# Kernel tuning notes

Measured on AMD Instinct MI355X. Metric: run time of the kernel, lower is better.

Reference implementation:

```python
import jax, jax.numpy as jnp
import numpy as np

BRANCH = 16   # children per internal node
DEPTH = 4     # levels 0..4, leaves at level 4
IN = 512
HID = 512

def _level_sizes():
    return [BRANCH ** d for d in range(DEPTH + 1)]

def setup_inputs() -> dict:
    key = jax.random.key(0)
    ks = jax.random.split(key, 9)
    N = sum(_level_sizes())  # 69905
    x = jax.random.normal(ks[0], (N, IN), dtype=jnp.float32)
    s = 1.0 / np.sqrt(IN + HID)  # torch nn.Linear default init bound
    def lin(kw, kb):
        w = jax.random.uniform(kw, (HID, IN + HID), jnp.float32, -s, s)
        b = jax.random.uniform(kb, (HID,), jnp.float32, -s, s)
        return w, b
    wi_w, wi_b = lin(ks[1], ks[2])
    wf_w, wf_b = lin(ks[3], ks[4])
    wo_w, wo_b = lin(ks[5], ks[6])
    wu_w, wu_b = lin(ks[7], ks[8])
    return {"x": x, "wi_w": wi_w, "wi_b": wi_b, "wf_w": wf_w, "wf_b": wf_b,
            "wo_w": wo_w, "wo_b": wo_b, "wu_w": wu_w, "wu_b": wu_b}

def reference(x, wi_w, wi_b, wf_w, wf_b, wo_w, wo_b, wu_w, wu_b):
    sizes = _level_sizes()
    offs = np.concatenate([[0], np.cumsum(sizes)])
    levels = [x[offs[d]:offs[d + 1]] for d in range(DEPTH + 1)]

    def gates(xh):
        i = jax.nn.sigmoid(xh @ wi_w.T + wi_b)
        o = jax.nn.sigmoid(xh @ wo_w.T + wo_b)
        u = jnp.tanh(xh @ wu_w.T + wu_b)
        return i, o, u

    # leaf_forward: h_prev = 0, no forget terms
    Xl = levels[DEPTH]
    xh = jnp.concatenate([Xl, jnp.zeros((Xl.shape[0], HID), Xl.dtype)], axis=1)
    i, o, u = gates(xh)
    C = i * u
    H = o * jnp.tanh(C)

    # node_forward, bottom-up. Faithful quirk of the source: the forget gate
    # is computed on the child CELL state (cat(x, c_k)), not the hidden state.
    for d in range(DEPTH - 1, -1, -1):
        Xd = levels[d]                      # [n, IN]
        n = Xd.shape[0]
        Hc = H.reshape(n, BRANCH, HID)      # children hidden
        Cc = C.reshape(n, BRANCH, HID)      # children cell
        h_sum = Hc.sum(axis=1)
        xh = jnp.concatenate([Xd, h_sum], axis=1)
        i, o, u = gates(xh)
        xc = jnp.concatenate([jnp.broadcast_to(Xd[:, None, :], (n, BRANCH, IN)), Cc], axis=-1)
        f = jax.nn.sigmoid(jnp.einsum('nbk,hk->nbh', xc, wf_w) + wf_b)
        C = i * u + (f * Cc).sum(axis=1)
        H = o * jnp.tanh(C)

    return H[0], C[0]
```

## Files before the change

### kernel.cpp

```cpp
#include <hip/hip_runtime.h>
#include <stdint.h>
#include <stddef.h>


typedef __bf16 bf16x8 __attribute__((ext_vector_type(8)));
typedef float  f32x4  __attribute__((ext_vector_type(4)));
typedef void __attribute__((address_space(3))) lds_void_t;
typedef void __attribute__((address_space(1))) gbl_void_t;

__device__ __forceinline__ uint16_t f2bf(float f) {
  union { __bf16 b; uint16_t u; } v;
  v.b = (__bf16)f;
  return v.u;
}
__device__ __forceinline__ float bf2f(uint16_t u) {
  union { uint32_t u; float f; } v; v.u = (uint32_t)u << 16;
  return v.f;
}
__device__ __forceinline__ float sig_(float x) {
  return __builtin_amdgcn_rcpf(1.0f + __expf(-x));
}
__device__ __forceinline__ float tanh_(float x) {
  return __builtin_fmaf(2.f,
      __builtin_amdgcn_rcpf(1.f + __expf(-2.f * x)), -1.f);
}

__global__ void k_conv_all(const float4* __restrict__ x,
                           ushort4* __restrict__ xdst, long n4x,
                           const float4* __restrict__ w0,
                           const float4* __restrict__ w1,
                           const float4* __restrict__ w2,
                           const float4* __restrict__ w3,
                           ushort4* __restrict__ wdst) {
  const long per4 = (long)512 * 1024 / 4;
  const long total = n4x + 4 * per4;
  long i = blockIdx.x * (long)blockDim.x + threadIdx.x;
  long stride = (long)gridDim.x * blockDim.x;
  for (; i < total; i += stride) {
    float4 v;
    ushort4* d;
    if (i < n4x) {
      v = x[i];
      d = xdst + i;
    } else {
      long j = i - n4x;
      long seg = j / per4, off2 = j - seg * per4;
      const float4* s = (seg == 0) ? w0 : (seg == 1) ? w1
                       : (seg == 2) ? w2 : w3;
      v = s[off2];
      d = wdst + j;
    }
    ushort4 r;
    r.x = f2bf(v.x); r.y = f2bf(v.y); r.z = f2bf(v.z); r.w = f2bf(v.w);
    *d = r;
  }
}

#define BM 128
#define BN 128
#define BK 32

__global__ __launch_bounds__(256, 3)
void k_leaf_fx(const uint16_t* __restrict__ Xleaf,
               const uint16_t* __restrict__ Wg,
               const float* __restrict__ bi, const float* __restrict__ bo,
               const float* __restrict__ bu,
               uint16_t* __restrict__ Cbf,
               const uint16_t* __restrict__ Xnext,
               uint16_t* __restrict__ xh_next,
               const uint16_t* __restrict__ Xbf,
               const uint16_t* __restrict__ Wf,
               float* __restrict__ FxAll) {
  __shared__ uint16_t smem[20480];
  const int tid = threadIdx.x, lane = tid & 63, wave = tid >> 6;
  const int lrow = lane & 15, quad = lane >> 4;

  if (blockIdx.x < 4096) {
    uint16_t* As = smem;
    uint16_t* Bs = smem + 8192;
    const int wm = (wave >> 1) * 64, wn = (wave & 1) * 32;
    long tm, tn;
    {
      int b = blockIdx.x;
      int x = b & 7, j = b >> 3, per = 64;
      tn = j & 7; tm = (long)x * per + (j >> 3);
    }
    f32x4 acc[3][4][2] = {};
    const int srow = lane >> 3;
    const int scol = (((lane & 7) ^ srow) << 3);
    const int rsw = lrow & 7;
    const int pc[2] = { ((0 + quad) ^ rsw) << 3, ((4 + quad) ^ rsw) << 3 };

    for (int k0 = 0; k0 < 512; k0 += 64) {
#pragma unroll
      for (int j = 0; j < 4; ++j) {
        int grp = wave * 4 + j;
        int row = grp * 8 + srow;
        const uint16_t* gp = Xleaf + (tm * 128 + row) * 512L + k0 + scol;
        __builtin_amdgcn_global_load_lds((gbl_void_t*)(uintptr_t)gp,
            (lds_void_t*)&As[grp * 512], 16, 0, 0);
      }
#pragma unroll
      for (int j = 0; j < 6; ++j) {
        int cc = wave * 6 + j;
        int g  = cc >> 3;
        long grow = (long)g * 512 + tn * 64 + (cc & 7) * 8 + srow;
        const uint16_t* gp = Wg + grow * 1024 + k0 + scol;
        __builtin_amdgcn_global_load_lds((gbl_void_t*)(uintptr_t)gp,
            (lds_void_t*)&Bs[cc * 512], 16, 0, 0);
      }
      __syncthreads();
#pragma unroll
      for (int h = 0; h < 2; ++h) {
        bf16x8 a[4];
#pragma unroll
        for (int f = 0; f < 4; ++f)
          a[f] = *(const bf16x8*)&As[(wm + f * 16 + lrow) * 64 + pc[h]];
#pragma unroll
        for (int g = 0; g < 3; ++g) {
          bf16x8 b0 = *(const bf16x8*)&Bs[(g * 64 + wn + lrow) * 64 + pc[h]];
          bf16x8 b1 = *(const bf16x8*)&Bs[(g * 64 + wn + 16 + lrow) * 64 +
                                          pc[h]];
#pragma unroll
          for (int fm = 0; fm < 4; ++fm) {
            acc[g][fm][0] = __builtin_amdgcn_mfma_f32_16x16x32_bf16(
                a[fm], b0, acc[g][fm][0], 0, 0, 0);
            acc[g][fm][1] = __builtin_amdgcn_mfma_f32_16x16x32_bf16(
                a[fm], b1, acc[g][fm][1], 0, 0, 0);
          }
        }
      }
      __syncthreads();
    }
#pragma unroll
    for (int fn = 0; fn < 2; ++fn) {
      long col = tn * 64 + wn + fn * 16 + lrow;
      float biv = bi[col], bov = bo[col], buv = bu[col];
#pragma unroll
      for (int fm = 0; fm < 4; ++fm) {
        long row0 = tm * 128 + wm + fm * 16 + quad * 4;
        long pg   = tm * 8 + (wm >> 4) + fm;
        float hs = 0.f;
#pragma unroll
        for (int r = 0; r < 4; ++r) {
          long row = row0 + r;
          float iv = sig_(acc[0][fm][fn][r] + biv);
          float ov = sig_(acc[1][fm][fn][r] + bov);
          float uv = tanh_(acc[2][fm][fn][r] + buv);
          float c  = iv * uv;
          Cbf[row * 512 + col] = f2bf(c);
          hs += ov * tanh_(c);
        }
        hs += __shfl_xor(hs, 16, 64);
        hs += __shfl_xor(hs, 32, 64);
        if (quad == 0) {
          xh_next[pg * 1024 + col]       = Xnext[pg * 512 + col];
          xh_next[pg * 1024 + 512 + col] = f2bf(hs);
        }
      }
    }
  } else {
    uint16_t* As = smem;
    uint16_t* Bs = smem + 4096;
    const int wm = (wave >> 1) * 64, wn = (wave & 1) * 64;
    int bid2 = (int)blockIdx.x - 4096;
    const long tm = bid2 % 35, tn = bid2 / 35;
    f32x4 acc[4][4] = {};
    const int srow2 = lane >> 2, scol2 = (lane & 3) * 8;
    for (int k0 = 0; k0 < 512; k0 += BK) {
#pragma unroll
      for (int i = 0; i < 2; ++i) {
        int row = i * 64 + wave * 16 + srow2;
        const uint16_t* gp = Xbf + (tm * BM + row) * 512L + k0 + scol2;
        __builtin_amdgcn_global_load_lds((gbl_void_t*)(uintptr_t)gp,
            (lds_void_t*)&As[i * 2048 + wave * 512], 16, 0, 0);
      }
#pragma unroll
      for (int i = 0; i < 2; ++i) {
        int row = i * 64 + wave * 16 + srow2;
        const uint16_t* gp = Wf + (tn * BN + row) * 1024L + k0 + scol2;
        __builtin_amdgcn_global_load_lds((gbl_void_t*)(uintptr_t)gp,
            (lds_void_t*)&Bs[i * 2048 + wave * 512], 16, 0, 0);
      }
      __syncthreads();
      bf16x8 a[4], b[4];
#pragma unroll
      for (int f = 0; f < 4; ++f)
        a[f] = *(const bf16x8*)&As[(wm + f * 16 + lrow) * BK + quad * 8];
#pragma unroll
      for (int f = 0; f < 4; ++f)
        b[f] = *(const bf16x8*)&Bs[(wn + f * 16 + lrow) * BK + quad * 8];
#pragma unroll
      for (int fm = 0; fm < 4; ++fm)
#pragma unroll
        for (int fn = 0; fn < 4; ++fn)
          acc[fm][fn] = __builtin_amdgcn_mfma_f32_16x16x32_bf16(
              a[fm], b[fn], acc[fm][fn], 0, 0, 0);
      __syncthreads();
    }
#pragma unroll
    for (int fm = 0; fm < 4; ++fm)
#pragma unroll
      for (int fn = 0; fn < 4; ++fn) {
        long col  = tn * BN + wn + fn * 16 + lrow;
        long row0 = tm * BM + wm + fm * 16 + quad * 4;
#pragma unroll
        for (int r = 0; r < 4; ++r)
          FxAll[(row0 + r) * 512 + col] = acc[fm][fn][r];
      }
  }
}

__global__ __launch_bounds__(256, 3)
void k_fc4_l3g(const uint16_t* __restrict__ Cbf,
               const uint16_t* __restrict__ Wfc,
               const float* __restrict__ Fx,
               const float* __restrict__ bfb,
               float* __restrict__ Fpart,
               const uint16_t* __restrict__ xhA,
               const uint16_t* __restrict__ Wg,
               float* __restrict__ G3) {
  __shared__ uint16_t smem[16384];
  const int tid = threadIdx.x, lane = tid & 63, wave = tid >> 6;
  const int lrow = lane & 15, quad = lane >> 4;
  const int srow = lane >> 3;
  const int scol = (((lane & 7) ^ srow) << 3);
  const int rsw = lrow & 7;
  const int pc[2] = { ((0 + quad) ^ rsw) << 3, ((4 + quad) ^ rsw) << 3 };

  if (blockIdx.x < 2048) {
    uint16_t* As = smem;
    uint16_t* Bs = smem + 8192;
    const int wm = (wave >> 1) * 64, wn = (wave & 1) * 64;
    long tm, tn;
    {
      int b = blockIdx.x;
      int x = b & 7, j = b >> 3, per = 64;
      tn = j & 3; tm = (long)x * per + (j >> 2);
    }
    f32x4 acc[4][4] = {};
    for (int k0 = 0; k0 < 512; k0 += 64) {
#pragma unroll
      for (int j = 0; j < 4; ++j) {
        int grp = wave * 4 + j;
        int row = grp * 8 + srow;
        const uint16_t* gp = Cbf + (tm * 128 + row) * 512L + k0 + scol;
        __builtin_amdgcn_global_load_lds((gbl_void_t*)(uintptr_t)gp,
            (lds_void_t*)&As[grp * 512], 16, 0, 0);
      }
#pragma unroll
      for (int j = 0; j < 4; ++j) {
        int row = wave * 32 + j * 8 + srow;
        const uint16_t* gp = Wfc + (tn * BN + row) * 1024L + k0 + scol;
        __builtin_amdgcn_global_load_lds((gbl_void_t*)(uintptr_t)gp,
            (lds_void_t*)&Bs[(wave * 32 + j * 8) * 64], 16, 0, 0);
      }
      __syncthreads();
#pragma unroll
      for (int h = 0; h < 2; ++h) {
        bf16x8 a[4], b[4];
#pragma unroll
        for (int f = 0; f < 4; ++f)
          a[f] = *(const bf16x8*)&As[(wm + f * 16 + lrow) * 64 + pc[h]];
#pragma unroll
        for (int f = 0; f < 4; ++f)
          b[f] = *(const bf16x8*)&Bs[(wn + f * 16 + lrow) * 64 + pc[h]];
#pragma unroll
        for (int fm = 0; fm < 4; ++fm)
#pragma unroll
          for (int fn = 0; fn < 4; ++fn)
            acc[fm][fn] = __builtin_amdgcn_mfma_f32_16x16x32_bf16(
                a[fm], b[fn], acc[fm][fn], 0, 0, 0);
      }
      __syncthreads();
    }
#pragma unroll
    for (int fm = 0; fm < 4; ++fm) {
      long pg   = tm * 8 + (wm >> 4) + fm;
      long row0 = tm * 128 + wm + fm * 16 + quad * 4;
#pragma unroll
      for (int fn = 0; fn < 4; ++fn) {
        long col = tn * BN + wn + fn * 16 + lrow;
        float fx = Fx[pg * 512 + col] + bfb[col];
        float t = 0.f;
#pragma unroll
        for (int r = 0; r < 4; ++r)
          t += sig_(fx + acc[fm][fn][r]) * bf2f(Cbf[(row0 + r) * 512 + col]);
        t += __shfl_xor(t, 16, 64);
        t += __shfl_xor(t, 32, 64);
        if (quad == 0) Fpart[pg * 512 + col] = t;
      }
    }
  } else {
    uint16_t* As = smem;
    uint16_t* Bs = smem + 4096;
    const int wm = (wave >> 1) * 32, wn = (wave & 1) * 32;
    long tm, tn;
    {
      int b = (int)blockIdx.x - 2048;
      int x = b & 7, j = b >> 3, per = 8;
      tn = j & 7; tm = (long)x * per + (j >> 3);
    }
    f32x4 acc[3][2][2] = {};
    for (int k0 = 0; k0 < 1024; k0 += 64) {
#pragma unroll
      for (int j = 0; j < 2; ++j) {
        int grp = wave * 2 + j;
        int row = grp * 8 + srow;
        const uint16_t* gp = xhA + (tm * 64 + row) * 1024L + k0 + scol;
        __builtin_amdgcn_global_load_lds((gbl_void_t*)(uintptr_t)gp,
            (lds_void_t*)&As[grp * 512], 16, 0, 0);
      }
#pragma unroll
      for (int j = 0; j < 6; ++j) {
        int cc = wave * 6 + j;
        int g  = cc >> 3;
        long grow = (long)g * 512 + tn * 64 + (cc & 7) * 8 + srow;
        const uint16_t* gp = Wg + grow * 1024 + k0 + scol;
        __builtin_amdgcn_global_load_lds((gbl_void_t*)(uintptr_t)gp,
            (lds_void_t*)&Bs[cc * 512], 16, 0, 0);
      }
      __syncthreads();
#pragma unroll
      for (int h = 0; h < 2; ++h) {
        bf16x8 a[2];
#pragma unroll
        for (int f = 0; f < 2; ++f)
          a[f] = *(const bf16x8*)&As[(wm + f * 16 + lrow) * 64 + pc[h]];
#pragma unroll
        for (int g = 0; g < 3; ++g) {
          bf16x8 b0 = *(const bf16x8*)&Bs[(g * 64 + wn + lrow) * 64 + pc[h]];
          bf16x8 b1 = *(const bf16x8*)&Bs[(g * 64 + wn + 16 + lrow) * 64 +
                                          pc[h]];
#pragma unroll
          for (int fm = 0; fm < 2; ++fm) {
            acc[g][fm][0] = __builtin_amdgcn_mfma_f32_16x16x32_bf16(
                a[fm], b0, acc[g][fm][0], 0, 0, 0);
            acc[g][fm][1] = __builtin_amdgcn_mfma_f32_16x16x32_bf16(
                a[fm], b1, acc[g][fm][1], 0, 0, 0);
          }
        }
      }
      __syncthreads();
    }
#pragma unroll
    for (int fn = 0; fn < 2; ++fn) {
      long col = tn * 64 + wn + fn * 16 + lrow;
#pragma unroll
      for (int fm = 0; fm < 2; ++fm) {
        long row0 = tm * 64 + wm + fm * 16 + quad * 4;
#pragma unroll
        for (int r = 0; r < 4; ++r) {
          long row = row0 + r;
#pragma unroll
          for (int g = 0; g < 3; ++g)
            G3[row * 1536 + g * 512 + col] = acc[g][fm][fn][r];
        }
      }
    }
  }
}

__global__ void k_level_final(const float* __restrict__ G3,
                              const float* __restrict__ Fpart,
                              const float* __restrict__ bi,
                              const float* __restrict__ bo,
                              const float* __restrict__ bu,
                              uint16_t* __restrict__ Cbf_out,
                              const uint16_t* __restrict__ Xnext,
                              uint16_t* __restrict__ xh_next) {
  const long p = blockIdx.x;
  const int hq = (threadIdx.x & 127) << 2;
  float4 b_i = *(const float4*)(bi + hq);
  float4 b_o = *(const float4*)(bo + hq);
  float4 b_u = *(const float4*)(bu + hq);
  const float* bip = &b_i.x; const float* bop = &b_o.x;
  const float* bup = &b_u.x;
  float hs[4] = {0.f, 0.f, 0.f, 0.f};
#pragma unroll 4
  for (int k = 0; k < 16; ++k) {
    long row = p * 16 + k;
    float4 gi = *(const float4*)(G3 + row * 1536 + hq);
    float4 go = *(const float4*)(G3 + row * 1536 + 512 + hq);
    float4 gu = *(const float4*)(G3 + row * 1536 + 1024 + hq);
    float4 fp = *(const float4*)(Fpart + row * 512 + hq);
    const float* gip = &gi.x; const float* gop = &go.x;
    const float* gup = &gu.x; const float* fpp = &fp.x;
    ushort4 cw; unsigned short* cwp = &cw.x;
#pragma unroll
    for (int j = 0; j < 4; ++j) {
      float iv = sig_(gip[j] + bip[j]);
      float ov = sig_(gop[j] + bop[j]);
      float uv = tanh_(gup[j] + bup[j]);
      float c  = iv * uv + fpp[j];
      cwp[j] = f2bf(c);
      hs[j] += ov * tanh_(c);
    }
    *(ushort4*)(Cbf_out + row * 512 + hq) = cw;
  }
  *(ushort4*)(xh_next + p * 1024 + hq) = *(const ushort4*)(Xnext + p * 512 + hq);
  ushort4 hw = {f2bf(hs[0]), f2bf(hs[1]), f2bf(hs[2]), f2bf(hs[3])};
  *(ushort4*)(xh_next + p * 1024 + 512 + hq) = hw;
}

__global__ __launch_bounds__(256, 3)
void k_fc2_l2g(const uint16_t* __restrict__ CbfU,
               const uint16_t* __restrict__ Wfc,
               const float* __restrict__ Fx,
               const float* __restrict__ bfb,
               float* __restrict__ Fpart,
               const uint16_t* __restrict__ xhB,
               const uint16_t* __restrict__ Wg,
               float* __restrict__ G3) {
  __shared__ uint16_t smem[16384];
  const int tid = threadIdx.x, lane = tid & 63, wave = tid >> 6;
  const int lrow = lane & 15, quad = lane >> 4;
  const int srow = lane >> 3;
  const int scol = (((lane & 7) ^ srow) << 3);
  const int rsw = lrow & 7;
  const int pc[2] = { ((0 + quad) ^ rsw) << 3, ((4 + quad) ^ rsw) << 3 };

  if (blockIdx.x < 256) {
    uint16_t* As = smem;
    uint16_t* Bs = smem + 4096;
    const int wm = (wave >> 1) * 32, wn = (wave & 1) * 64;
    long tm, tn;
    {
      int b = blockIdx.x;
      int x = b & 7, j = b >> 3, per = 8;
      tn = j & 3; tm = (long)x * per + (j >> 2);
    }
    f32x4 acc[2][4] = {};
    for (int k0 = 0; k0 < 512; k0 += 64) {
#pragma unroll
      for (int j = 0; j < 2; ++j) {
        int grp = wave * 2 + j;
        int row = grp * 8 + srow;
        const uint16_t* gp = CbfU + (tm * 64 + row) * 512L + k0 + scol;
        __builtin_amdgcn_global_load_lds((gbl_void_t*)(uintptr_t)gp,
            (lds_void_t*)&As[grp * 512], 16, 0, 0);
      }
#pragma unroll
      for (int j = 0; j < 4; ++j) {
        int row = wave * 32 + j * 8 + srow;
        const uint16_t* gp = Wfc + (tn * BN + row) * 1024L + k0 + scol;
        __builtin_amdgcn_global_load_lds((gbl_void_t*)(uintptr_t)gp,
            (lds_void_t*)&Bs[(wave * 32 + j * 8) * 64], 16, 0, 0);
      }
      __syncthreads();
#pragma unroll
      for (int h = 0; h < 2; ++h) {
        bf16x8 a[2], b[4];
#pragma unroll
        for (int f = 0; f < 2; ++f)
          a[f] = *(const bf16x8*)&As[(wm + f * 16 + lrow) * 64 + pc[h]];
#pragma unroll
        for (int f = 0; f < 4; ++f)
          b[f] = *(const bf16x8*)&Bs[(wn + f * 16 + lrow) * 64 + pc[h]];
#pragma unroll
        for (int fm = 0; fm < 2; ++fm)
#pragma unroll
          for (int fn = 0; fn < 4; ++fn)
            acc[fm][fn] = __builtin_amdgcn_mfma_f32_16x16x32_bf16(
                a[fm], b[fn], acc[fm][fn], 0, 0, 0);
      }
      __syncthreads();
    }
#pragma unroll
    for (int fm = 0; fm < 2; ++fm) {
      long pg   = tm * 4 + (wm >> 4) + fm;
      long row0 = tm * 64 + wm + fm * 16 + quad * 4;
#pragma unroll
      for (int fn = 0; fn < 4; ++fn) {
        long col = tn * BN + wn + fn * 16 + lrow;
        float fx = Fx[pg * 512 + col] + bfb[col];
        float t = 0.f;
#pragma unroll
        for (int r = 0; r < 4; ++r)
          t += sig_(fx + acc[fm][fn][r]) * bf2f(CbfU[(row0 + r) * 512 + col]);
        t += __shfl_xor(t, 16, 64);
        t += __shfl_xor(t, 32, 64);
        if (quad == 0) Fpart[pg * 512 + col] = t;
      }
    }
  } else {
    uint16_t* As = smem;
    uint16_t* Bs = smem + 4096;
    const int wm = (wave >> 1) * 32, wn = (wave & 1) * 32;
    int b = (int)blockIdx.x - 256;
    long tm = b >> 3, tn = b & 7;
    f32x4 acc[3][2][2] = {};
    for (int k0 = 0; k0 < 1024; k0 += 64) {
#pragma unroll
      for (int j = 0; j < 2; ++j) {
        int grp = wave * 2 + j;
        int row = grp * 8 + srow;
        const uint16_t* gp = xhB + (tm * 64 + row) * 1024L + k0 + scol;
        __builtin_amdgcn_global_load_lds((gbl_void_t*)(uintptr_t)gp,
            (lds_void_t*)&As[grp * 512], 16, 0, 0);
      }
#pragma unroll
      for (int j = 0; j < 6; ++j) {
        int cc = wave * 6 + j;
        int g  = cc >> 3;
        long grow = (long)g * 512 + tn * 64 + (cc & 7) * 8 + srow;
        const uint16_t* gp = Wg + grow * 1024 + k0 + scol;
        __builtin_amdgcn_global_load_lds((gbl_void_t*)(uintptr_t)gp,
            (lds_void_t*)&Bs[cc * 512], 16, 0, 0);
      }
      __syncthreads();
#pragma unroll
      for (int h = 0; h < 2; ++h) {
        bf16x8 a[2];
#pragma unroll
        for (int f = 0; f < 2; ++f)
          a[f] = *(const bf16x8*)&As[(wm + f * 16 + lrow) * 64 + pc[h]];
#pragma unroll
        for (int g = 0; g < 3; ++g) {
          bf16x8 b0 = *(const bf16x8*)&Bs[(g * 64 + wn + lrow) * 64 + pc[h]];
          bf16x8 b1 = *(const bf16x8*)&Bs[(g * 64 + wn + 16 + lrow) * 64 +
                                          pc[h]];
#pragma unroll
          for (int fm = 0; fm < 2; ++fm) {
            acc[g][fm][0] = __builtin_amdgcn_mfma_f32_16x16x32_bf16(
                a[fm], b0, acc[g][fm][0], 0, 0, 0);
            acc[g][fm][1] = __builtin_amdgcn_mfma_f32_16x16x32_bf16(
                a[fm], b1, acc[g][fm][1], 0, 0, 0);
          }
        }
      }
      __syncthreads();
    }
#pragma unroll
    for (int fn = 0; fn < 2; ++fn) {
      long col = tn * 64 + wn + fn * 16 + lrow;
#pragma unroll
      for (int fm = 0; fm < 2; ++fm) {
        long row0 = tm * 64 + wm + fm * 16 + quad * 4;
#pragma unroll
        for (int r = 0; r < 4; ++r) {
          long row = row0 + r;
#pragma unroll
          for (int g = 0; g < 3; ++g)
            G3[row * 1536 + g * 512 + col] = acc[g][fm][fn][r];
        }
      }
    }
  }
}

__global__ __launch_bounds__(256)
void k_fcdot(const uint16_t* __restrict__ Cbf,
             const uint16_t* __restrict__ Wfc,
             const float* __restrict__ Fx,
             const float* __restrict__ bfb,
             float* __restrict__ Fpart,
             const uint16_t* __restrict__ xhC,
             const uint16_t* __restrict__ Wg,
             float* __restrict__ Gf) {
  __shared__ uint16_t smem[12288];
  const int tid = threadIdx.x, lane = tid & 63, wave = tid >> 6;
  if (blockIdx.x < 16) {
    uint16_t* As = smem;
    uint16_t* Bs = smem + 4096;
    const int lrow = lane & 15, quad = lane >> 4;
    const int wm = (wave >> 1) * 32, wn = (wave & 1) * 64;
    int b = blockIdx.x;
    long tm = b >> 2, tn = b & 3;
    f32x4 acc[2][4] = {};
    const int srow = lane >> 3;
    const int scol = (((lane & 7) ^ srow) << 3);
    const int rsw = lrow & 7;
    const int pc[2] = { ((0 + quad) ^ rsw) << 3, ((4 + quad) ^ rsw) << 3 };
    for (int k0 = 0; k0 < 512; k0 += 64) {
#pragma unroll
      for (int j = 0; j < 2; ++j) {
        int grp = wave * 2 + j;
        int row = grp * 8 + srow;
        const uint16_t* gp = Cbf + (tm * 64 + row) * 512L + k0 + scol;
        __builtin_amdgcn_global_load_lds((gbl_void_t*)(uintptr_t)gp,
            (lds_void_t*)&As[grp * 512], 16, 0, 0);
      }
#pragma unroll
      for (int j = 0; j < 4; ++j) {
        int row = wave * 32 + j * 8 + srow;
        const uint16_t* gp = Wfc + (tn * 128 + row) * 1024L + k0 + scol;
        __builtin_amdgcn_global_load_lds((gbl_void_t*)(uintptr_t)gp,
            (lds_void_t*)&Bs[(wave * 32 + j * 8) * 64], 16, 0, 0);
      }
      __syncthreads();
#pragma unroll
      for (int h = 0; h < 2; ++h) {
        bf16x8 a[2], bb[4];
#pragma unroll
        for (int f = 0; f < 2; ++f)
          a[f] = *(const bf16x8*)&As[(wm + f * 16 + lrow) * 64 + pc[h]];
#pragma unroll
        for (int f = 0; f < 4; ++f)
          bb[f] = *(const bf16x8*)&Bs[(wn + f * 16 + lrow) * 64 + pc[h]];
#pragma unroll
        for (int fm = 0; fm < 2; ++fm)
#pragma unroll
          for (int fn = 0; fn < 4; ++fn)
            acc[fm][fn] = __builtin_amdgcn_mfma_f32_16x16x32_bf16(
                a[fm], bb[fn], acc[fm][fn], 0, 0, 0);
      }
      __syncthreads();
    }
#pragma unroll
    for (int fm = 0; fm < 2; ++fm) {
      long pg   = tm * 4 + (wm >> 4) + fm;
      long row0 = tm * 64 + wm + fm * 16 + quad * 4;
#pragma unroll
      for (int fn = 0; fn < 4; ++fn) {
        long col = tn * 128 + wn + fn * 16 + lrow;
        float fx = Fx[pg * 512 + col] + bfb[col];
        float t = 0.f;
#pragma unroll
        for (int r = 0; r < 4; ++r)
          t += sig_(fx + acc[fm][fn][r]) * bf2f(Cbf[(row0 + r) * 512 + col]);
        t += __shfl_xor(t, 16, 64);
        t += __shfl_xor(t, 32, 64);
        if (quad == 0) Fpart[pg * 512 + col] = t;
      }
    }
  } else {
    int wid = (int)(((long)(blockIdx.x - 16) * 256 + tid) >> 6);
    if (wid >= 16 * 1536) return;
    int m = wid / 1536, n = wid - m * 1536;
    const uint16_t* a = xhC + (long)m * 1024;
    const uint16_t* b = Wg + (long)n * 1024;
    int k0 = lane * 16;
    float s = 0.f;
#pragma unroll
    for (int j = 0; j < 16; j += 4) {
      ushort4 av = *(const ushort4*)(a + k0 + j);
      ushort4 bv = *(const ushort4*)(b + k0 + j);
      s += bf2f(av.x) * bf2f(bv.x) + bf2f(av.y) * bf2f(bv.y)
         + bf2f(av.z) * bf2f(bv.z) + bf2f(av.w) * bf2f(bv.w);
    }
#pragma unroll
    for (int off = 32; off; off >>= 1) s += __shfl_xor(s, off, 64);
    if (lane == 0) Gf[(long)m * 1536 + n] = s;
  }
}

__global__ void k_dot_merge(const uint16_t* __restrict__ xhC,
                            const uint16_t* __restrict__ Wg,
                            float* __restrict__ Gf,
                            const float* __restrict__ CupA,
                            const float* __restrict__ WfF,
                            float* __restrict__ Fc) {
  int wid  = (int)((blockIdx.x * (long)blockDim.x + threadIdx.x) >> 6);
  int lane = threadIdx.x & 63;
  if (wid < 1536) {
    const uint16_t* a = xhC;
    const uint16_t* b = Wg + (long)wid * 1024;
    int k0 = lane * 16;
    float s = 0.f;
#pragma unroll
    for (int j = 0; j < 16; j += 4) {
      ushort4 av = *(const ushort4*)(a + k0 + j);
      ushort4 bv = *(const ushort4*)(b + k0 + j);
      s += bf2f(av.x) * bf2f(bv.x) + bf2f(av.y) * bf2f(bv.y)
         + bf2f(av.z) * bf2f(bv.z) + bf2f(av.w) * bf2f(bv.w);
    }
#pragma unroll
    for (int off = 32; off; off >>= 1) s += __shfl_xor(s, off, 64);
    if (lane == 0) Gf[wid] = s;
  } else {
    int w2 = wid - 1536;
    if (w2 >= 16 * 512) return;
    int m = w2 >> 9, n = w2 & 511;
    const float* a = CupA + (long)m * 512;
    const float* b = WfF + (long)n * 1024;
    int k0 = lane * 8;
    float s = 0.f;
#pragma unroll
    for (int j = 0; j < 8; j += 4) {
      float4 av = *(const float4*)(a + k0 + j);
      float4 bv = *(const float4*)(b + k0 + j);
      s += av.x * bv.x + av.y * bv.y + av.z * bv.z + av.w * bv.w;
    }
#pragma unroll
    for (int off = 32; off; off >>= 1) s += __shfl_xor(s, off, 64);
    if (lane == 0) Fc[(long)m * 512 + n] = s;
  }
}

__global__ __launch_bounds__(1024)
void k_lvl1_tail(const float* __restrict__ G,
                 const float* __restrict__ Fpart,
                 const float* __restrict__ bi,
                 const float* __restrict__ bo,
                 const float* __restrict__ bu,
                 float* __restrict__ Cv,
                 const uint16_t* __restrict__ xroot,
                 uint16_t* __restrict__ xh) {
  __shared__ float Hl[16 * 512];
  const int tid = threadIdx.x;
#pragma unroll
  for (int it = 0; it < 2; ++it) {
    int idx = it * 1024 + tid;
    int p = idx >> 7, hq = (idx & 127) << 2;
    const float* g = G + (long)p * 1536;
    float4 gi = *(const float4*)(g + hq);
    float4 go = *(const float4*)(g + 512 + hq);
    float4 gu = *(const float4*)(g + 1024 + hq);
    float4 b_i = *(const float4*)(bi + hq);
    float4 b_o = *(const float4*)(bo + hq);
    float4 b_u = *(const float4*)(bu + hq);
    float4 fp = *(const float4*)(Fpart + (long)p * 512 + hq);
    const float* gip = &gi.x; const float* gop = &go.x;
    const float* gup = &gu.x; const float* bip = &b_i.x;
    const float* bop = &b_o.x; const float* bup = &b_u.x;
    const float* fpp = &fp.x;
    float4 hv, cv;
    float* hvp = &hv.x; float* cvp = &cv.x;
#pragma unroll
    for (int j = 0; j < 4; ++j) {
      float iv = sig_(gip[j] + bip[j]);
      float ov = sig_(gop[j] + bop[j]);
      float uv = tanh_(gup[j] + bup[j]);
      float c  = iv * uv + fpp[j];
      cvp[j] = c;
      hvp[j] = ov * tanh_(c);
    }
    *(float4*)(Cv + (long)p * 512 + hq) = cv;
    *(float4*)(&Hl[p * 512 + hq]) = hv;
  }
  __syncthreads();
  if (tid < 128) {
    int hq = tid << 2;
    float4 s = {0.f, 0.f, 0.f, 0.f};
#pragma unroll
    for (int b = 0; b < 16; ++b) {
      float4 v = *(const float4*)(&Hl[b * 512 + hq]);
      s.x += v.x; s.y += v.y; s.z += v.z; s.w += v.w;
    }
    *(ushort4*)(xh + hq) = *(const ushort4*)(xroot + hq);
    ushort4 hw = {f2bf(s.x), f2bf(s.y), f2bf(s.z), f2bf(s.w)};
    *(ushort4*)(xh + 512 + hq) = hw;
  }
}

__global__ void k_root_tail(const float* __restrict__ Fc,
                            const float* __restrict__ Fx,
                            const float* __restrict__ bfb,
                            const float* __restrict__ Cc,
                            const float* __restrict__ G,
                            const float* __restrict__ bi,
                            const float* __restrict__ bo,
                            const float* __restrict__ bu,
                            float* __restrict__ H, float* __restrict__ Cv) {
  int hq = (threadIdx.x & 127) << 2;
  float4 fxv = *(const float4*)(Fx + hq);
  float4 bfv = *(const float4*)(bfb + hq);
  float fx0 = fxv.x + bfv.x, fx1 = fxv.y + bfv.y;
  float fx2 = fxv.z + bfv.z, fx3 = fxv.w + bfv.w;
  float a0 = 0.f, a1 = 0.f, a2 = 0.f, a3 = 0.f;
#pragma unroll 4
  for (int b = 0; b < 16; ++b) {
    float4 f = *(const float4*)(Fc + (long)b * 512 + hq);
    float4 c = *(const float4*)(Cc + (long)b * 512 + hq);
    a0 += sig_(fx0 + f.x) * c.x;
    a1 += sig_(fx1 + f.y) * c.y;
    a2 += sig_(fx2 + f.z) * c.z;
    a3 += sig_(fx3 + f.w) * c.w;
  }
  float fpp[4] = {a0, a1, a2, a3};
  float4 gi = *(const float4*)(G + hq);
  float4 go = *(const float4*)(G + 512 + hq);
  float4 gu = *(const float4*)(G + 1024 + hq);
  float4 b_i = *(const float4*)(bi + hq);
  float4 b_o = *(const float4*)(bo + hq);
  float4 b_u = *(const float4*)(bu + hq);
  const float* gip = &gi.x; const float* gop = &go.x; const float* gup = &gu.x;
  const float* bip = &b_i.x; const float* bop = &b_o.x; const float* bup = &b_u.x;
  float4 hv, cv;
  float* hvp = &hv.x; float* cvp = &cv.x;
#pragma unroll
  for (int j = 0; j < 4; ++j) {
    float iv = sig_(gip[j] + bip[j]);
    float ov = sig_(gop[j] + bop[j]);
    float uv = tanh_(gup[j] + bup[j]);
    float c  = iv * uv + fpp[j];
    cvp[j] = c;
    hvp[j] = ov * tanh_(c);
  }
  *(float4*)(H  + hq) = hv;
  *(float4*)(Cv + hq) = cv;
}

extern "C" void kernel_launch(void* const* d_in, const int* in_sizes, int n_in,
                              void* d_out, int out_size, void* d_ws, size_t ws_size,
                              hipStream_t stream) {
  const float* x    = (const float*)d_in[0];
  const float* wi_w = (const float*)d_in[1];
  const float* wi_b = (const float*)d_in[2];
  const float* wf_w = (const float*)d_in[3];
  const float* wf_b = (const float*)d_in[4];
  const float* wo_w = (const float*)d_in[5];
  const float* wo_b = (const float*)d_in[6];
  const float* wu_w = (const float*)d_in[7];
  const float* wu_b = (const float*)d_in[8];
  (void)in_sizes; (void)n_in; (void)out_size; (void)ws_size;

  static const long offs[5] = {0, 1, 17, 273, 4369};
  const long NTOT = 69905;

  char* ws = (char*)d_ws;
  size_t off = 0;
  auto alloc = [&](size_t bytes) -> void* {
    void* p = ws + off;
    off += (bytes + 255) & ~(size_t)255;
    return p;
  };
  uint16_t* Xbf   = (uint16_t*)alloc(NTOT * 512 * 2);
  uint16_t* Wgw   = (uint16_t*)alloc((size_t)2048 * 1024 * 2);
  uint16_t* Wg    = Wgw;
  uint16_t* Wf    = Wgw + (size_t)1536 * 1024;
  float*    FxAll = (float*)alloc((size_t)4480 * 512 * 4);
  uint16_t* Cbf   = (uint16_t*)alloc((size_t)65536 * 512 * 2);
  uint16_t* CbfU  = (uint16_t*)alloc((size_t)4096 * 512 * 2);
  uint16_t* CbfU2 = (uint16_t*)alloc((size_t)256 * 512 * 2);
  uint16_t* xhA   = (uint16_t*)alloc((size_t)4096 * 1024 * 2);
  uint16_t* xhB   = (uint16_t*)alloc((size_t)256 * 1024 * 2);
  uint16_t* xhC   = (uint16_t*)alloc((size_t)16 * 1024 * 2);
  float*    Fpart = (float*)alloc((size_t)4096 * 512 * 4);
  float*    G3    = (float*)alloc((size_t)4096 * 1536 * 4);
  float*    Gf    = (float*)alloc((size_t)16 * 1536 * 4);
  float*    Fc    = (float*)alloc((size_t)16 * 512 * 4);
  float*    CupA  = (float*)alloc((size_t)16 * 512 * 4);

  {
    long n4x = NTOT * 512 / 4;
    k_conv_all<<<8192, 256, 0, stream>>>(
        (const float4*)x, (ushort4*)Xbf, n4x,
        (const float4*)wi_w, (const float4*)wo_w,
        (const float4*)wu_w, (const float4*)wf_w, (ushort4*)Wgw);
  }

  k_leaf_fx<<<4236, 256, 0, stream>>>(
      Xbf + offs[4] * 512, Wg, wi_b, wo_b, wu_b,
      Cbf, Xbf + offs[3] * 512, xhA,
      Xbf, Wf, FxAll);

  k_fc4_l3g<<<2560, 256, 0, stream>>>(
      Cbf, Wf + 512, FxAll + offs[3] * 512, wf_b, Fpart,
      xhA, Wg, G3);

  k_level_final<<<256, 128, 0, stream>>>(
      G3, Fpart, wi_b, wo_b, wu_b, CbfU, Xbf + offs[2] * 512, xhB);

  k_fc2_l2g<<<288, 256, 0, stream>>>(
      CbfU, Wf + 512, FxAll + offs[2] * 512, wf_b, Fpart,
      xhB, Wg, G3);

  k_level_final<<<16, 128, 0, stream>>>(
      G3, Fpart, wi_b, wo_b, wu_b, CbfU2, Xbf + offs[1] * 512, xhC);

  k_fcdot<<<6160, 256, 0, stream>>>(CbfU2, Wf + 512,
                                    FxAll + offs[1] * 512, wf_b, Fpart,
                                    xhC, Wg, Gf);

  k_lvl1_tail<<<1, 1024, 0, stream>>>(Gf, Fpart, wi_b, wo_b, wu_b,
                                      CupA, Xbf + offs[0] * 512, xhC);

  {
    long waves = 1536 + 16L * 512;
    k_dot_merge<<<(int)(waves / 4), 256, 0, stream>>>(
        xhC, Wg, Gf, CupA, wf_w + 512, Fc);
  }
  k_root_tail<<<1, 128, 0, stream>>>(Fc, FxAll, wf_b, CupA, Gf,
                                     wi_b, wo_b, wu_b,
                                     (float*)d_out, (float*)d_out + 512);
}
```

Before: 473.1 us.

## Fuse upper tree levels into one persistent kernel with grid barriers

Replaces the chain of eight small kernels for levels 3..0 with a single persistent kernel of 768 blocks. Software grid barriers built on atomics separate the phases, and each phase's work is distributed over the blocks in grid-stride form. This is meant to remove the launch overhead and tail idle time between the many tiny dependent kernels. In exchange it adds barrier spin costs, and it relies on all 768 blocks being co-resident under a normal launch. If they are not, the barrier can deadlock, though the spin limit eventually breaks the wait.

```diff
diff --git a/kernel.cpp b/kernel.cpp
--- a/kernel.cpp
+++ b/kernel.cpp
@@ -23,6 +23,32 @@
 __device__ __forceinline__ float tanh_(float x) {
   return __builtin_fmaf(2.f,
       __builtin_amdgcn_rcpf(1.f + __expf(-2.f * x)), -1.f);
+}
+
+#define NBLK 768u
+__device__ __forceinline__ void gbar(unsigned* bar) {
+  __syncthreads();
+  if (threadIdx.x == 0) {
+    __threadfence();
+    unsigned g = __hip_atomic_load(bar + 1, __ATOMIC_RELAXED,
+                                   __HIP_MEMORY_SCOPE_AGENT);
+    unsigned a = __hip_atomic_fetch_add(bar, 1u, __ATOMIC_ACQ_REL,
+                                        __HIP_MEMORY_SCOPE_AGENT) + 1u;
+    if (a == NBLK) {
+      __hip_atomic_store(bar, 0u, __ATOMIC_RELAXED, __HIP_MEMORY_SCOPE_AGENT);
+      __hip_atomic_fetch_add(bar + 1, 1u, __ATOMIC_RELEASE,
+                             __HIP_MEMORY_SCOPE_AGENT);
+    } else {
+      long spins = 0;
+      while (__hip_atomic_load(bar + 1, __ATOMIC_ACQUIRE,
+                               __HIP_MEMORY_SCOPE_AGENT) == g) {
+        if (++spins > (1L << 28)) break;
+        __builtin_amdgcn_s_sleep(8);
+      }
+    }
+    __threadfence();
+  }
+  __syncthreads();
 }
 
 __global__ void k_conv_all(const float4* __restrict__ x,
@@ -211,166 +237,34 @@
   }
 }
 
-__global__ __launch_bounds__(256, 3)
-void k_fc4_l3g(const uint16_t* __restrict__ Cbf,
-               const uint16_t* __restrict__ Wfc,
-               const float* __restrict__ Fx,
-               const float* __restrict__ bfb,
-               float* __restrict__ Fpart,
-               const uint16_t* __restrict__ xhA,
-               const uint16_t* __restrict__ Wg,
-               float* __restrict__ G3) {
-  __shared__ uint16_t smem[16384];
-  const int tid = threadIdx.x, lane = tid & 63, wave = tid >> 6;
-  const int lrow = lane & 15, quad = lane >> 4;
-  const int srow = lane >> 3;
-  const int scol = (((lane & 7) ^ srow) << 3);
-  const int rsw = lrow & 7;
-  const int pc[2] = { ((0 + quad) ^ rsw) << 3, ((4 + quad) ^ rsw) << 3 };
-
-  if (blockIdx.x < 2048) {
-    uint16_t* As = smem;
-    uint16_t* Bs = smem + 8192;
-    const int wm = (wave >> 1) * 64, wn = (wave & 1) * 64;
-    long tm, tn;
-    {
-      int b = blockIdx.x;
-      int x = b & 7, j = b >> 3, per = 64;
-      tn = j & 3; tm = (long)x * per + (j >> 2);
-    }
-    f32x4 acc[4][4] = {};
-    for (int k0 = 0; k0 < 512; k0 += 64) {
-#pragma unroll
-      for (int j = 0; j < 4; ++j) {
-        int grp = wave * 4 + j;
-        int row = grp * 8 + srow;
-        const uint16_t* gp = Cbf + (tm * 128 + row) * 512L + k0 + scol;
-        __builtin_amdgcn_global_load_lds((gbl_void_t*)(uintptr_t)gp,
-            (lds_void_t*)&As[grp * 512], 16, 0, 0);
-      }
-#pragma unroll
-      for (int j = 0; j < 4; ++j) {
-        int row = wave * 32 + j * 8 + srow;
-        const uint16_t* gp = Wfc + (tn * BN + row) * 1024L + k0 + scol;
-        __builtin_amdgcn_global_load_lds((gbl_void_t*)(uintptr_t)gp,
-            (lds_void_t*)&Bs[(wave * 32 + j * 8) * 64], 16, 0, 0);
-      }
-      __syncthreads();
-#pragma unroll
-      for (int h = 0; h < 2; ++h) {
-        bf16x8 a[4], b[4];
-#pragma unroll
-        for (int f = 0; f < 4; ++f)
-          a[f] = *(const bf16x8*)&As[(wm + f * 16 + lrow) * 64 + pc[h]];
-#pragma unroll
-        for (int f = 0; f < 4; ++f)
-          b[f] = *(const bf16x8*)&Bs[(wn + f * 16 + lrow) * 64 + pc[h]];
-#pragma unroll
-        for (int fm = 0; fm < 4; ++fm)
-#pragma unroll
-          for (int fn = 0; fn < 4; ++fn)
-            acc[fm][fn] = __builtin_amdgcn_mfma_f32_16x16x32_bf16(
-                a[fm], b[fn], acc[fm][fn], 0, 0, 0);
-      }
-      __syncthreads();
-    }
-#pragma unroll
-    for (int fm = 0; fm < 4; ++fm) {
-      long pg   = tm * 8 + (wm >> 4) + fm;
-      long row0 = tm * 128 + wm + fm * 16 + quad * 4;
-#pragma unroll
-      for (int fn = 0; fn < 4; ++fn) {
-        long col = tn * BN + wn + fn * 16 + lrow;
-        float fx = Fx[pg * 512 + col] + bfb[col];
-        float t = 0.f;
-#pragma unroll
-        for (int r = 0; r < 4; ++r)
-          t += sig_(fx + acc[fm][fn][r]) * bf2f(Cbf[(row0 + r) * 512 + col]);
-        t += __shfl_xor(t, 16, 64);
-        t += __shfl_xor(t, 32, 64);
-        if (quad == 0) Fpart[pg * 512 + col] = t;
-      }
-    }
-  } else {
-    uint16_t* As = smem;
-    uint16_t* Bs = smem + 4096;
-    const int wm = (wave >> 1) * 32, wn = (wave & 1) * 32;
-    long tm, tn;
-    {
-      int b = (int)blockIdx.x - 2048;
-      int x = b & 7, j = b >> 3, per = 8;
-      tn = j & 7; tm = (long)x * per + (j >> 3);
-    }
-    f32x4 acc[3][2][2] = {};
-    for (int k0 = 0; k0 < 1024; k0 += 64) {
-#pragma unroll
-      for (int j = 0; j < 2; ++j) {
-        int grp = wave * 2 + j;
-        int row = grp * 8 + srow;
-        const uint16_t* gp = xhA + (tm * 64 + row) * 1024L + k0 + scol;
-        __builtin_amdgcn_global_load_lds((gbl_void_t*)(uintptr_t)gp,
-            (lds_void_t*)&As[grp * 512], 16, 0, 0);
-      }
-#pragma unroll
-      for (int j = 0; j < 6; ++j) {
-        int cc = wave * 6 + j;
-        int g  = cc >> 3;
-        long grow = (long)g * 512 + tn * 64 + (cc & 7) * 8 + srow;
-        const uint16_t* gp = Wg + grow * 1024 + k0 + scol;
-        __builtin_amdgcn_global_load_lds((gbl_void_t*)(uintptr_t)gp,
-            (lds_void_t*)&Bs[cc * 512], 16, 0, 0);
-      }
-      __syncthreads();
-#pragma unroll
-      for (int h = 0; h < 2; ++h) {
-        bf16x8 a[2];
-#pragma unroll
-        for (int f = 0; f < 2; ++f)
-          a[f] = *(const bf16x8*)&As[(wm + f * 16 + lrow) * 64 + pc[h]];
-#pragma unroll
-        for (int g = 0; g < 3; ++g) {
-          bf16x8 b0 = *(const bf16x8*)&Bs[(g * 64 + wn + lrow) * 64 + pc[h]];
-          bf16x8 b1 = *(const bf16x8*)&Bs[(g * 64 + wn + 16 + lrow) * 64 +
-                                          pc[h]];
-#pragma unroll
-          for (int fm = 0; fm < 2; ++fm) {
-            acc[g][fm][0] = __builtin_amdgcn_mfma_f32_16x16x32_bf16(
-                a[fm], b0, acc[g][fm][0], 0, 0, 0);
-            acc[g][fm][1] = __builtin_amdgcn_mfma_f32_16x16x32_bf16(
-                a[fm], b1, acc[g][fm][1], 0, 0, 0);
-          }
-        }
-      }
-      __syncthreads();
-    }
-#pragma unroll
-    for (int fn = 0; fn < 2; ++fn) {
-      long col = tn * 64 + wn + fn * 16 + lrow;
-#pragma unroll
-      for (int fm = 0; fm < 2; ++fm) {
-        long row0 = tm * 64 + wm + fm * 16 + quad * 4;
-#pragma unroll
-        for (int r = 0; r < 4; ++r) {
-          long row = row0 + r;
-#pragma unroll
-          for (int g = 0; g < 3; ++g)
-            G3[row * 1536 + g * 512 + col] = acc[g][fm][fn][r];
-        }
-      }
-    }
-  }
-}
-
-__global__ void k_level_final(const float* __restrict__ G3,
-                              const float* __restrict__ Fpart,
-                              const float* __restrict__ bi,
-                              const float* __restrict__ bo,
-                              const float* __restrict__ bu,
-                              uint16_t* __restrict__ Cbf_out,
-                              const uint16_t* __restrict__ Xnext,
-                              uint16_t* __restrict__ xh_next) {
-  const long p = blockIdx.x;
-  const int hq = (threadIdx.x & 127) << 2;
+struct CoopArgs {
+  const uint16_t* Cbf;
+  const uint16_t* Wfc;
+  const float*    FxAll;
+  const float*    bfb;
+  float*          Fpart;
+  const uint16_t* xhA;
+  const uint16_t* Wg;
+  float*          G3;
+  const float*    bi; const float* bo; const float* bu;
+  uint16_t*       CbfU;
+  const uint16_t* Xbf;
+  uint16_t*       xhB;
+  uint16_t*       CbfU2;
+  uint16_t*       xhC;
+  float*          Gf;
+  float*          CupA;
+  const float*    WfF;
+  float*          Fc;
+  float*          H; float* Cv;
+  unsigned*       bar;
+};
+
+__device__ __forceinline__ void level_final_body(
+    int p, int tid, const float* G3, const float* Fpart,
+    const float* bi, const float* bo, const float* bu,
+    uint16_t* Cbf_out, const uint16_t* Xnext, uint16_t* xh_next) {
+  const int hq = (tid & 127) << 2;
   float4 b_i = *(const float4*)(bi + hq);
   float4 b_o = *(const float4*)(bo + hq);
   float4 b_u = *(const float4*)(bu + hq);
@@ -379,7 +273,7 @@
   float hs[4] = {0.f, 0.f, 0.f, 0.f};
 #pragma unroll 4
   for (int k = 0; k < 16; ++k) {
-    long row = p * 16 + k;
+    long row = (long)p * 16 + k;
     float4 gi = *(const float4*)(G3 + row * 1536 + hq);
     float4 go = *(const float4*)(G3 + row * 1536 + 512 + hq);
     float4 gu = *(const float4*)(G3 + row * 1536 + 1024 + hq);
@@ -398,21 +292,16 @@
     }
     *(ushort4*)(Cbf_out + row * 512 + hq) = cw;
   }
-  *(ushort4*)(xh_next + p * 1024 + hq) = *(const ushort4*)(Xnext + p * 512 + hq);
+  *(ushort4*)(xh_next + (long)p * 1024 + hq) =
+      *(const ushort4*)(Xnext + (long)p * 512 + hq);
   ushort4 hw = {f2bf(hs[0]), f2bf(hs[1]), f2bf(hs[2]), f2bf(hs[3])};
-  *(ushort4*)(xh_next + p * 1024 + 512 + hq) = hw;
+  *(ushort4*)(xh_next + (long)p * 1024 + 512 + hq) = hw;
 }
 
 __global__ __launch_bounds__(256, 3)
-void k_fc2_l2g(const uint16_t* __restrict__ CbfU,
-               const uint16_t* __restrict__ Wfc,
-               const float* __restrict__ Fx,
-               const float* __restrict__ bfb,
-               float* __restrict__ Fpart,
-               const uint16_t* __restrict__ xhB,
-               const uint16_t* __restrict__ Wg,
-               float* __restrict__ G3) {
-  __shared__ uint16_t smem[16384];
+void k_coop(CoopArgs a) {
+  __shared__ __align__(16) unsigned char smem_raw[40960];
+  uint16_t* smem = (uint16_t*)smem_raw;
   const int tid = threadIdx.x, lane = tid & 63, wave = tid >> 6;
   const int lrow = lane & 15, quad = lane >> 4;
   const int srow = lane >> 3;
@@ -420,301 +309,478 @@
   const int rsw = lrow & 7;
   const int pc[2] = { ((0 + quad) ^ rsw) << 3, ((4 + quad) ^ rsw) << 3 };
 
-  if (blockIdx.x < 256) {
-    uint16_t* As = smem;
-    uint16_t* Bs = smem + 4096;
-    const int wm = (wave >> 1) * 32, wn = (wave & 1) * 64;
-    long tm, tn;
-    {
-      int b = blockIdx.x;
-      int x = b & 7, j = b >> 3, per = 8;
-      tn = j & 3; tm = (long)x * per + (j >> 2);
-    }
-    f32x4 acc[2][4] = {};
-    for (int k0 = 0; k0 < 512; k0 += 64) {
-#pragma unroll
-      for (int j = 0; j < 2; ++j) {
-        int grp = wave * 2 + j;
-        int row = grp * 8 + srow;
-        const uint16_t* gp = CbfU + (tm * 64 + row) * 512L + k0 + scol;
-        __builtin_amdgcn_global_load_lds((gbl_void_t*)(uintptr_t)gp,
-            (lds_void_t*)&As[grp * 512], 16, 0, 0);
-      }
+  for (int job = blockIdx.x; job < 2560; job += NBLK) {
+    if (job < 2048) {
+      uint16_t* As = smem;
+      uint16_t* Bs = smem + 8192;
+      const int wm = (wave >> 1) * 64, wn = (wave & 1) * 64;
+      long tm, tn;
+      {
+        int b = job;
+        int x = b & 7, j = b >> 3, per = 64;
+        tn = j & 3; tm = (long)x * per + (j >> 2);
+      }
+      f32x4 acc[4][4] = {};
+      for (int k0 = 0; k0 < 512; k0 += 64) {
+#pragma unroll
+        for (int j = 0; j < 4; ++j) {
+          int grp = wave * 4 + j;
+          int row = grp * 8 + srow;
+          const uint16_t* gp = a.Cbf + (tm * 128 + row) * 512L + k0 + scol;
+          __builtin_amdgcn_global_load_lds((gbl_void_t*)(uintptr_t)gp,
+              (lds_void_t*)&As[grp * 512], 16, 0, 0);
+        }
+#pragma unroll
+        for (int j = 0; j < 4; ++j) {
+          int row = wave * 32 + j * 8 + srow;
+          const uint16_t* gp = a.Wfc + (tn * BN + row) * 1024L + k0 + scol;
+          __builtin_amdgcn_global_load_lds((gbl_void_t*)(uintptr_t)gp,
+              (lds_void_t*)&Bs[(wave * 32 + j * 8) * 64], 16, 0, 0);
+        }
+        __syncthreads();
+#pragma unroll
+        for (int h = 0; h < 2; ++h) {
+          bf16x8 av[4], bv[4];
+#pragma unroll
+          for (int f = 0; f < 4; ++f)
+            av[f] = *(const bf16x8*)&As[(wm + f * 16 + lrow) * 64 + pc[h]];
+#pragma unroll
+          for (int f = 0; f < 4; ++f)
+            bv[f] = *(const bf16x8*)&Bs[(wn + f * 16 + lrow) * 64 + pc[h]];
+#pragma unroll
+          for (int fm = 0; fm < 4; ++fm)
+#pragma unroll
+            for (int fn = 0; fn < 4; ++fn)
+              acc[fm][fn] = __builtin_amdgcn_mfma_f32_16x16x32_bf16(
+                  av[fm], bv[fn], acc[fm][fn], 0, 0, 0);
+        }
+        __syncthreads();
+      }
+#pragma unroll
+      for (int fm = 0; fm < 4; ++fm) {
+        long pg   = tm * 8 + (wm >> 4) + fm;
+        long row0 = tm * 128 + wm + fm * 16 + quad * 4;
+#pragma unroll
+        for (int fn = 0; fn < 4; ++fn) {
+          long col = tn * BN + wn + fn * 16 + lrow;
+          float fx = a.FxAll[(273 + pg) * 512 + col] + a.bfb[col];
+          float t = 0.f;
+#pragma unroll
+          for (int r = 0; r < 4; ++r)
+            t += sig_(fx + acc[fm][fn][r]) *
+                 bf2f(a.Cbf[(row0 + r) * 512 + col]);
+          t += __shfl_xor(t, 16, 64);
+          t += __shfl_xor(t, 32, 64);
+          if (quad == 0) a.Fpart[pg * 512 + col] = t;
+        }
+      }
+    } else {
+      uint16_t* As = smem;
+      uint16_t* Bs = smem + 4096;
+      const int wm = (wave >> 1) * 32, wn = (wave & 1) * 32;
+      long tm, tn;
+      {
+        int b = job - 2048;
+        int x = b & 7, j = b >> 3, per = 8;
+        tn = j & 7; tm = (long)x * per + (j >> 3);
+      }
+      f32x4 acc[3][2][2] = {};
+      for (int k0 = 0; k0 < 1024; k0 += 64) {
+#pragma unroll
+        for (int j = 0; j < 2; ++j) {
+          int grp = wave * 2 + j;
+          int row = grp * 8 + srow;
+          const uint16_t* gp = a.xhA + (tm * 64 + row) * 1024L + k0 + scol;
+          __builtin_amdgcn_global_load_lds((gbl_void_t*)(uintptr_t)gp,
+              (lds_void_t*)&As[grp * 512], 16, 0, 0);
+        }
+#pragma unroll
+        for (int j = 0; j < 6; ++j) {
+          int cc = wave * 6 + j;
+          int g  = cc >> 3;
+          long grow = (long)g * 512 + tn * 64 + (cc & 7) * 8 + srow;
+          const uint16_t* gp = a.Wg + grow * 1024 + k0 + scol;
+          __builtin_amdgcn_global_load_lds((gbl_void_t*)(uintptr_t)gp,
+              (lds_void_t*)&Bs[cc * 512], 16, 0, 0);
+        }
+        __syncthreads();
+#pragma unroll
+        for (int h = 0; h < 2; ++h) {
+          bf16x8 av[2];
+#pragma unroll
+          for (int f = 0; f < 2; ++f)
+            av[f] = *(const bf16x8*)&As[(wm + f * 16 + lrow) * 64 + pc[h]];
+#pragma unroll
+          for (int g = 0; g < 3; ++g) {
+            bf16x8 b0 = *(const bf16x8*)&Bs[(g * 64 + wn + lrow) * 64 +
+                                            pc[h]];
+            bf16x8 b1 = *(const bf16x8*)&Bs[(g * 64 + wn + 16 + lrow) * 64 +
+                                            pc[h]];
+#pragma unroll
+            for (int fm = 0; fm < 2; ++fm) {
+              acc[g][fm][0] = __builtin_amdgcn_mfma_f32_16x16x32_bf16(
+                  av[fm], b0, acc[g][fm][0], 0, 0, 0);
+              acc[g][fm][1] = __builtin_amdgcn_mfma_f32_16x16x32_bf16(
+                  av[fm], b1, acc[g][fm][1], 0, 0, 0);
+            }
+          }
+        }
+        __syncthreads();
+      }
+#pragma unroll
+      for (int fn = 0; fn < 2; ++fn) {
+        long col = tn * 64 + wn + fn * 16 + lrow;
+#pragma unroll
+        for (int fm = 0; fm < 2; ++fm) {
+          long row0 = tm * 64 + wm + fm * 16 + quad * 4;
+#pragma unroll
+          for (int r = 0; r < 4; ++r) {
+            long row = row0 + r;
+#pragma unroll
+            for (int g = 0; g < 3; ++g)
+              a.G3[row * 1536 + g * 512 + col] = acc[g][fm][fn][r];
+          }
+        }
+      }
+    }
+  }
+  gbar(a.bar);
+
+  if (blockIdx.x < 256 && tid < 128)
+    level_final_body(blockIdx.x, tid, a.G3, a.Fpart, a.bi, a.bo, a.bu,
+                     a.CbfU, a.Xbf + 17 * 512, a.xhB);
+  gbar(a.bar);
+
+  if (blockIdx.x < 288) {
+    int job = blockIdx.x;
+    if (job < 256) {
+      uint16_t* As = smem;
+      uint16_t* Bs = smem + 4096;
+      const int wm = (wave >> 1) * 32, wn = (wave & 1) * 64;
+      long tm, tn;
+      {
+        int b = job;
+        int x = b & 7, j = b >> 3, per = 8;
+        tn = j & 3; tm = (long)x * per + (j >> 2);
+      }
+      f32x4 acc[2][4] = {};
+      for (int k0 = 0; k0 < 512; k0 += 64) {
+#pragma unroll
+        for (int j = 0; j < 2; ++j) {
+          int grp = wave * 2 + j;
+          int row = grp * 8 + srow;
+          const uint16_t* gp = a.CbfU + (tm * 64 + row) * 512L + k0 + scol;
+          __builtin_amdgcn_global_load_lds((gbl_void_t*)(uintptr_t)gp,
+              (lds_void_t*)&As[grp * 512], 16, 0, 0);
+        }
+#pragma unroll
+        for (int j = 0; j < 4; ++j) {
+          int row = wave * 32 + j * 8 + srow;
+          const uint16_t* gp = a.Wfc + (tn * BN + row) * 1024L + k0 + scol;
+          __builtin_amdgcn_global_load_lds((gbl_void_t*)(uintptr_t)gp,
+              (lds_void_t*)&Bs[(wave * 32 + j * 8) * 64], 16, 0, 0);
+        }
+        __syncthreads();
+#pragma unroll
+        for (int h = 0; h < 2; ++h) {
+          bf16x8 av[2], bv[4];
+#pragma unroll
+          for (int f = 0; f < 2; ++f)
+            av[f] = *(const bf16x8*)&As[(wm + f * 16 + lrow) * 64 + pc[h]];
+#pragma unroll
+          for (int f = 0; f < 4; ++f)
+            bv[f] = *(const bf16x8*)&Bs[(wn + f * 16 + lrow) * 64 + pc[h]];
+#pragma unroll
+          for (int fm = 0; fm < 2; ++fm)
+#pragma unroll
+            for (int fn = 0; fn < 4; ++fn)
+              acc[fm][fn] = __builtin_amdgcn_mfma_f32_16x16x32_bf16(
+                  av[fm], bv[fn], acc[fm][fn], 0, 0, 0);
+        }
+        __syncthreads();
+      }
+#pragma unroll
+      for (int fm = 0; fm < 2; ++fm) {
+        long pg   = tm * 4 + (wm >> 4) + fm;
+        long row0 = tm * 64 + wm + fm * 16 + quad * 4;
+#pragma unroll
+        for (int fn = 0; fn < 4; ++fn) {
+          long col = tn * BN + wn + fn * 16 + lrow;
+          float fx = a.FxAll[(17 + pg) * 512 + col] + a.bfb[col];
+          float t = 0.f;
+#pragma unroll
+          for (int r = 0; r < 4; ++r)
+            t += sig_(fx + acc[fm][fn][r]) *
+                 bf2f(a.CbfU[(row0 + r) * 512 + col]);
+          t += __shfl_xor(t, 16, 64);
+          t += __shfl_xor(t, 32, 64);
+          if (quad == 0) a.Fpart[pg * 512 + col] = t;
+        }
+      }
+    } else {
+      uint16_t* As = smem;
+      uint16_t* Bs = smem + 4096;
+      const int wm = (wave >> 1) * 32, wn = (wave & 1) * 32;
+      int b = job - 256;
+      long tm = b >> 3, tn = b & 7;
+      f32x4 acc[3][2][2] = {};
+      for (int k0 = 0; k0 < 1024; k0 += 64) {
+#pragma unroll
+        for (int j = 0; j < 2; ++j) {
+          int grp = wave * 2 + j;
+          int row = grp * 8 + srow;
+          const uint16_t* gp = a.xhB + (tm * 64 + row) * 1024L + k0 + scol;
+          __builtin_amdgcn_global_load_lds((gbl_void_t*)(uintptr_t)gp,
+              (lds_void_t*)&As[grp * 512], 16, 0, 0);
+        }
+#pragma unroll
+        for (int j = 0; j < 6; ++j) {
+          int cc = wave * 6 + j;
+          int g  = cc >> 3;
+          long grow = (long)g * 512 + tn * 64 + (cc & 7) * 8 + srow;
+          const uint16_t* gp = a.Wg + grow * 1024 + k0 + scol;
+          __builtin_amdgcn_global_load_lds((gbl_void_t*)(uintptr_t)gp,
+              (lds_void_t*)&Bs[cc * 512], 16, 0, 0);
+        }
+        __syncthreads();
+#pragma unroll
+        for (int h = 0; h < 2; ++h) {
+          bf16x8 av[2];
+#pragma unroll
+          for (int f = 0; f < 2; ++f)
+            av[f] = *(const bf16x8*)&As[(wm + f * 16 + lrow) * 64 + pc[h]];
+#pragma unroll
+          for (int g = 0; g < 3; ++g) {
+            bf16x8 b0 = *(const bf16x8*)&Bs[(g * 64 + wn + lrow) * 64 +
+                                            pc[h]];
+            bf16x8 b1 = *(const bf16x8*)&Bs[(g * 64 + wn + 16 + lrow) * 64 +
+                                            pc[h]];
+#pragma unroll
+            for (int fm = 0; fm < 2; ++fm) {
+              acc[g][fm][0] = __builtin_amdgcn_mfma_f32_16x16x32_bf16(
+                  av[fm], b0, acc[g][fm][0], 0, 0, 0);
+              acc[g][fm][1] = __builtin_amdgcn_mfma_f32_16x16x32_bf16(
+                  av[fm], b1, acc[g][fm][1], 0, 0, 0);
+            }
+          }
+        }
+        __syncthreads();
+      }
+#pragma unroll
+      for (int fn = 0; fn < 2; ++fn) {
+        long col = tn * 64 + wn + fn * 16 + lrow;
+#pragma unroll
+        for (int fm = 0; fm < 2; ++fm) {
+          long row0 = tm * 64 + wm + fm * 16 + quad * 4;
+#pragma unroll
+          for (int r = 0; r < 4; ++r) {
+            long row = row0 + r;
+#pragma unroll
+            for (int g = 0; g < 3; ++g)
+              a.G3[row * 1536 + g * 512 + col] = acc[g][fm][fn][r];
+          }
+        }
+      }
+    }
+  }
+  gbar(a.bar);
+
+  if (blockIdx.x < 16 && tid < 128)
+    level_final_body(blockIdx.x, tid, a.G3, a.Fpart, a.bi, a.bo, a.bu,
+                     a.CbfU2, a.Xbf + 1 * 512, a.xhC);
+  gbar(a.bar);
+
+  for (int job = blockIdx.x; job < 6160; job += NBLK) {
+    if (job < 16) {
+      uint16_t* As = smem;
+      uint16_t* Bs = smem + 4096;
+      const int wm = (wave >> 1) * 32, wn = (wave & 1) * 64;
+      long tm = job >> 2, tn = job & 3;
+      f32x4 acc[2][4] = {};
+      for (int k0 = 0; k0 < 512; k0 += 64) {
+#pragma unroll
+        for (int j = 0; j < 2; ++j) {
+          int grp = wave * 2 + j;
+          int row = grp * 8 + srow;
+          const uint16_t* gp = a.CbfU2 + (tm * 64 + row) * 512L + k0 + scol;
+          __builtin_amdgcn_global_load_lds((gbl_void_t*)(uintptr_t)gp,
+              (lds_void_t*)&As[grp * 512], 16, 0, 0);
+        }
+#pragma unroll
+        for (int j = 0; j < 4; ++j) {
+          int row = wave * 32 + j * 8 + srow;
+          const uint16_t* gp = a.Wfc + (tn * 128 + row) * 1024L + k0 + scol;
+          __builtin_amdgcn_global_load_lds((gbl_void_t*)(uintptr_t)gp,
+              (lds_void_t*)&Bs[(wave * 32 + j * 8) * 64], 16, 0, 0);
+        }
+        __syncthreads();
+#pragma unroll
+        for (int h = 0; h < 2; ++h) {
+          bf16x8 av[2], bv[4];
+#pragma unroll
+          for (int f = 0; f < 2; ++f)
+            av[f] = *(const bf16x8*)&As[(wm + f * 16 + lrow) * 64 + pc[h]];
+#pragma unroll
+          for (int f = 0; f < 4; ++f)
+            bv[f] = *(const bf16x8*)&Bs[(wn + f * 16 + lrow) * 64 + pc[h]];
+#pragma unroll
+          for (int fm = 0; fm < 2; ++fm)
+#pragma unroll
+            for (int fn = 0; fn < 4; ++fn)
+              acc[fm][fn] = __builtin_amdgcn_mfma_f32_16x16x32_bf16(
+                  av[fm], bv[fn], acc[fm][fn], 0, 0, 0);
+        }
+        __syncthreads();
+      }
+#pragma unroll
+      for (int fm = 0; fm < 2; ++fm) {
+        long pg   = tm * 4 + (wm >> 4) + fm;
+        long row0 = tm * 64 + wm + fm * 16 + quad * 4;
+#pragma unroll
+        for (int fn = 0; fn < 4; ++fn) {
+          long col = tn * 128 + wn + fn * 16 + lrow;
+          float fx = a.FxAll[(1 + pg) * 512 + col] + a.bfb[col];
+          float t = 0.f;
+#pragma unroll
+          for (int r = 0; r < 4; ++r)
+            t += sig_(fx + acc[fm][fn][r]) *
+                 bf2f(a.CbfU2[(row0 + r) * 512 + col]);
+          t += __shfl_xor(t, 16, 64);
+          t += __shfl_xor(t, 32, 64);
+          if (quad == 0) a.Fpart[pg * 512 + col] = t;
+        }
+      }
+    } else {
+      int wid = (job - 16) * 4 + wave;
+      int m = wid / 1536, n = wid - m * 1536;
+      const uint16_t* ap = a.xhC + (long)m * 1024;
+      const uint16_t* bp = a.Wg + (long)n * 1024;
+      int k0 = lane * 16;
+      float s = 0.f;
+#pragma unroll
+      for (int j = 0; j < 16; j += 4) {
+        ushort4 avv = *(const ushort4*)(ap + k0 + j);
+        ushort4 bvv = *(const ushort4*)(bp + k0 + j);
+        s += bf2f(avv.x) * bf2f(bvv.x) + bf2f(avv.y) * bf2f(bvv.y)
+           + bf2f(avv.z) * bf2f(bvv.z) + bf2f(avv.w) * bf2f(bvv.w);
+      }
+#pragma unroll
+      for (int off = 32; off; off >>= 1) s += __shfl_xor(s, off, 64);
+      if (lane == 0) a.Gf[(long)m * 1536 + n] = s;
+    }
+  }
+  gbar(a.bar);
+
+  if (blockIdx.x == 0) {
+    float* Hl = (float*)smem_raw;
+    for (int it = 0; it < 8; ++it) {
+      int idx = it * 256 + tid;
+      int p = idx >> 7, hq = (idx & 127) << 2;
+      const float* g = a.Gf + (long)p * 1536;
+      float4 gi = *(const float4*)(g + hq);
+      float4 go = *(const float4*)(g + 512 + hq);
+      float4 gu = *(const float4*)(g + 1024 + hq);
+      float4 b_i = *(const float4*)(a.bi + hq);
+      float4 b_o = *(const float4*)(a.bo + hq);
+      float4 b_u = *(const float4*)(a.bu + hq);
+      float4 fp = *(const float4*)(a.Fpart + (long)p * 512 + hq);
+      const float* gip = &gi.x; const float* gop = &go.x;
+      const float* gup = &gu.x; const float* bip = &b_i.x;
+      const float* bop = &b_o.x; const float* bup = &b_u.x;
+      const float* fpp = &fp.x;
+      float4 hv, cv;
+      float* hvp = &hv.x; float* cvp = &cv.x;
 #pragma unroll
       for (int j = 0; j < 4; ++j) {
-        int row = wave * 32 + j * 8 + srow;
-        const uint16_t* gp = Wfc + (tn * BN + row) * 1024L + k0 + scol;
-        __builtin_amdgcn_global_load_lds((gbl_void_t*)(uintptr_t)gp,
-            (lds_void_t*)&Bs[(wave * 32 + j * 8) * 64], 16, 0, 0);
-      }
-      __syncthreads();
-#pragma unroll
-      for (int h = 0; h < 2; ++h) {
-        bf16x8 a[2], b[4];
-#pragma unroll
-        for (int f = 0; f < 2; ++f)
-          a[f] = *(const bf16x8*)&As[(wm + f * 16 + lrow) * 64 + pc[h]];
-#pragma unroll
-        for (int f = 0; f < 4; ++f)
-          b[f] = *(const bf16x8*)&Bs[(wn + f * 16 + lrow) * 64 + pc[h]];
-#pragma unroll
-        for (int fm = 0; fm < 2; ++fm)
-#pragma unroll
-          for (int fn = 0; fn < 4; ++fn)
-            acc[fm][fn] = __builtin_amdgcn_mfma_f32_16x16x32_bf16(
-                a[fm], b[fn], acc[fm][fn], 0, 0, 0);
-      }
-      __syncthreads();
-    }
-#pragma unroll
-    for (int fm = 0; fm < 2; ++fm) {
-      long pg   = tm * 4 + (wm >> 4) + fm;
-      long row0 = tm * 64 + wm + fm * 16 + quad * 4;
-#pragma unroll
-      for (int fn = 0; fn < 4; ++fn) {
-        long col = tn * BN + wn + fn * 16 + lrow;
-        float fx = Fx[pg * 512 + col] + bfb[col];
-        float t = 0.f;
-#pragma unroll
-        for (int r = 0; r < 4; ++r)
-          t += sig_(fx + acc[fm][fn][r]) * bf2f(CbfU[(row0 + r) * 512 + col]);
-        t += __shfl_xor(t, 16, 64);
-        t += __shfl_xor(t, 32, 64);
-        if (quad == 0) Fpart[pg * 512 + col] = t;
-      }
-    }
-  } else {
-    uint16_t* As = smem;
-    uint16_t* Bs = smem + 4096;
-    const int wm = (wave >> 1) * 32, wn = (wave & 1) * 32;
-    int b = (int)blockIdx.x - 256;
-    long tm = b >> 3, tn = b & 7;
-    f32x4 acc[3][2][2] = {};
-    for (int k0 = 0; k0 < 1024; k0 += 64) {
-#pragma unroll
-      for (int j = 0; j < 2; ++j) {
-        int grp = wave * 2 + j;
-        int row = grp * 8 + srow;
-        const uint16_t* gp = xhB + (tm * 64 + row) * 1024L + k0 + scol;
-        __builtin_amdgcn_global_load_lds((gbl_void_t*)(uintptr_t)gp,
-            (lds_void_t*)&As[grp * 512], 16, 0, 0);
-      }
-#pragma unroll
-      for (int j = 0; j < 6; ++j) {
-        int cc = wave * 6 + j;
-        int g  = cc >> 3;
-        long grow = (long)g * 512 + tn * 64 + (cc & 7) * 8 + srow;
-        const uint16_t* gp = Wg + grow * 1024 + k0 + scol;
-        __builtin_amdgcn_global_load_lds((gbl_void_t*)(uintptr_t)gp,
-            (lds_void_t*)&Bs[cc * 512], 16, 0, 0);
-      }
-      __syncthreads();
-#pragma unroll
-      for (int h = 0; h < 2; ++h) {
-        bf16x8 a[2];
-#pragma unroll
-        for (int f = 0; f < 2; ++f)
-          a[f] = *(const bf16x8*)&As[(wm + f * 16 + lrow) * 64 + pc[h]];
-#pragma unroll
-        for (int g = 0; g < 3; ++g) {
-          bf16x8 b0 = *(const bf16x8*)&Bs[(g * 64 + wn + lrow) * 64 + pc[h]];
-          bf16x8 b1 = *(const bf16x8*)&Bs[(g * 64 + wn + 16 + lrow) * 64 +
-                                          pc[h]];
-#pragma unroll
-          for (int fm = 0; fm < 2; ++fm) {
-            acc[g][fm][0] = __builtin_amdgcn_mfma_f32_16x16x32_bf16(
-                a[fm], b0, acc[g][fm][0], 0, 0, 0);
-            acc[g][fm][1] = __builtin_amdgcn_mfma_f32_16x16x32_bf16(
-                a[fm], b1, acc[g][fm][1], 0, 0, 0);
-          }
-        }
-      }
-      __syncthreads();
-    }
-#pragma unroll
-    for (int fn = 0; fn < 2; ++fn) {
-      long col = tn * 64 + wn + fn * 16 + lrow;
-#pragma unroll
-      for (int fm = 0; fm < 2; ++fm) {
-        long row0 = tm * 64 + wm + fm * 16 + quad * 4;
-#pragma unroll
-        for (int r = 0; r < 4; ++r) {
-          long row = row0 + r;
-#pragma unroll
-          for (int g = 0; g < 3; ++g)
-            G3[row * 1536 + g * 512 + col] = acc[g][fm][fn][r];
-        }
-      }
-    }
-  }
-}
-
-__global__ __launch_bounds__(256)
-void k_fcdot(const uint16_t* __restrict__ Cbf,
-             const uint16_t* __restrict__ Wfc,
-             const float* __restrict__ Fx,
-             const float* __restrict__ bfb,
-             float* __restrict__ Fpart,
-             const uint16_t* __restrict__ xhC,
-             const uint16_t* __restrict__ Wg,
-             float* __restrict__ Gf) {
-  __shared__ uint16_t smem[12288];
-  const int tid = threadIdx.x, lane = tid & 63, wave = tid >> 6;
-  if (blockIdx.x < 16) {
-    uint16_t* As = smem;
-    uint16_t* Bs = smem + 4096;
-    const int lrow = lane & 15, quad = lane >> 4;
-    const int wm = (wave >> 1) * 32, wn = (wave & 1) * 64;
-    int b = blockIdx.x;
-    long tm = b >> 2, tn = b & 3;
-    f32x4 acc[2][4] = {};
-    const int srow = lane >> 3;
-    const int scol = (((lane & 7) ^ srow) << 3);
-    const int rsw = lrow & 7;
-    const int pc[2] = { ((0 + quad) ^ rsw) << 3, ((4 + quad) ^ rsw) << 3 };
-    for (int k0 = 0; k0 < 512; k0 += 64) {
-#pragma unroll
-      for (int j = 0; j < 2; ++j) {
-        int grp = wave * 2 + j;
-        int row = grp * 8 + srow;
-        const uint16_t* gp = Cbf + (tm * 64 + row) * 512L + k0 + scol;
-        __builtin_amdgcn_global_load_lds((gbl_void_t*)(uintptr_t)gp,
-            (lds_void_t*)&As[grp * 512], 16, 0, 0);
-      }
-#pragma unroll
-      for (int j = 0; j < 4; ++j) {
-        int row = wave * 32 + j * 8 + srow;
-        const uint16_t* gp = Wfc + (tn * 128 + row) * 1024L + k0 + scol;
-        __builtin_amdgcn_global_load_lds((gbl_void_t*)(uintptr_t)gp,
-            (lds_void_t*)&Bs[(wave * 32 + j * 8) * 64], 16, 0, 0);
-      }
-      __syncthreads();
-#pragma unroll
-      for (int h = 0; h < 2; ++h) {
-        bf16x8 a[2], bb[4];
-#pragma unroll
-        for (int f = 0; f < 2; ++f)
-          a[f] = *(const bf16x8*)&As[(wm + f * 16 + lrow) * 64 + pc[h]];
-#pragma unroll
-        for (int f = 0; f < 4; ++f)
-          bb[f] = *(const bf16x8*)&Bs[(wn + f * 16 + lrow) * 64 + pc[h]];
-#pragma unroll
-        for (int fm = 0; fm < 2; ++fm)
-#pragma unroll
-          for (int fn = 0; fn < 4; ++fn)
-            acc[fm][fn] = __builtin_amdgcn_mfma_f32_16x16x32_bf16(
-                a[fm], bb[fn], acc[fm][fn], 0, 0, 0);
-      }
-      __syncthreads();
-    }
-#pragma unroll
-    for (int fm = 0; fm < 2; ++fm) {
-      long pg   = tm * 4 + (wm >> 4) + fm;
-      long row0 = tm * 64 + wm + fm * 16 + quad * 4;
-#pragma unroll
-      for (int fn = 0; fn < 4; ++fn) {
-        long col = tn * 128 + wn + fn * 16 + lrow;
-        float fx = Fx[pg * 512 + col] + bfb[col];
-        float t = 0.f;
-#pragma unroll
-        for (int r = 0; r < 4; ++r)
-          t += sig_(fx + acc[fm][fn][r]) * bf2f(Cbf[(row0 + r) * 512 + col]);
-        t += __shfl_xor(t, 16, 64);
-        t += __shfl_xor(t, 32, 64);
-        if (quad == 0) Fpart[pg * 512 + col] = t;
-      }
-    }
-  } else {
-    int wid = (int)(((long)(blockIdx.x - 16) * 256 + tid) >> 6);
-    if (wid >= 16 * 1536) return;
-    int m = wid / 1536, n = wid - m * 1536;
-    const uint16_t* a = xhC + (long)m * 1024;
-    const uint16_t* b = Wg + (long)n * 1024;
-    int k0 = lane * 16;
-    float s = 0.f;
-#pragma unroll
-    for (int j = 0; j < 16; j += 4) {
-      ushort4 av = *(const ushort4*)(a + k0 + j);
-      ushort4 bv = *(const ushort4*)(b + k0 + j);
-      s += bf2f(av.x) * bf2f(bv.x) + bf2f(av.y) * bf2f(bv.y)
-         + bf2f(av.z) * bf2f(bv.z) + bf2f(av.w) * bf2f(bv.w);
-    }
-#pragma unroll
-    for (int off = 32; off; off >>= 1) s += __shfl_xor(s, off, 64);
-    if (lane == 0) Gf[(long)m * 1536 + n] = s;
-  }
-}
-
-__global__ void k_dot_merge(const uint16_t* __restrict__ xhC,
-                            const uint16_t* __restrict__ Wg,
-                            float* __restrict__ Gf,
-                            const float* __restrict__ CupA,
-                            const float* __restrict__ WfF,
-                            float* __restrict__ Fc) {
-  int wid  = (int)((blockIdx.x * (long)blockDim.x + threadIdx.x) >> 6);
-  int lane = threadIdx.x & 63;
-  if (wid < 1536) {
-    const uint16_t* a = xhC;
-    const uint16_t* b = Wg + (long)wid * 1024;
-    int k0 = lane * 16;
-    float s = 0.f;
-#pragma unroll
-    for (int j = 0; j < 16; j += 4) {
-      ushort4 av = *(const ushort4*)(a + k0 + j);
-      ushort4 bv = *(const ushort4*)(b + k0 + j);
-      s += bf2f(av.x) * bf2f(bv.x) + bf2f(av.y) * bf2f(bv.y)
-         + bf2f(av.z) * bf2f(bv.z) + bf2f(av.w) * bf2f(bv.w);
-    }
-#pragma unroll
-    for (int off = 32; off; off >>= 1) s += __shfl_xor(s, off, 64);
-    if (lane == 0) Gf[wid] = s;
-  } else {
-    int w2 = wid - 1536;
-    if (w2 >= 16 * 512) return;
-    int m = w2 >> 9, n = w2 & 511;
-    const float* a = CupA + (long)m * 512;
-    const float* b = WfF + (long)n * 1024;
-    int k0 = lane * 8;
-    float s = 0.f;
-#pragma unroll
-    for (int j = 0; j < 8; j += 4) {
-      float4 av = *(const float4*)(a + k0 + j);
-      float4 bv = *(const float4*)(b + k0 + j);
-      s += av.x * bv.x + av.y * bv.y + av.z * bv.z + av.w * bv.w;
-    }
-#pragma unroll
-    for (int off = 32; off; off >>= 1) s += __shfl_xor(s, off, 64);
-    if (lane == 0) Fc[(long)m * 512 + n] = s;
-  }
-}
-
-__global__ __launch_bounds__(1024)
-void k_lvl1_tail(const float* __restrict__ G,
-                 const float* __restrict__ Fpart,
-                 const float* __restrict__ bi,
-                 const float* __restrict__ bo,
-                 const float* __restrict__ bu,
-                 float* __restrict__ Cv,
-                 const uint16_t* __restrict__ xroot,
-                 uint16_t* __restrict__ xh) {
-  __shared__ float Hl[16 * 512];
-  const int tid = threadIdx.x;
-#pragma unroll
-  for (int it = 0; it < 2; ++it) {
-    int idx = it * 1024 + tid;
-    int p = idx >> 7, hq = (idx & 127) << 2;
-    const float* g = G + (long)p * 1536;
-    float4 gi = *(const float4*)(g + hq);
-    float4 go = *(const float4*)(g + 512 + hq);
-    float4 gu = *(const float4*)(g + 1024 + hq);
-    float4 b_i = *(const float4*)(bi + hq);
-    float4 b_o = *(const float4*)(bo + hq);
-    float4 b_u = *(const float4*)(bu + hq);
-    float4 fp = *(const float4*)(Fpart + (long)p * 512 + hq);
+        float iv = sig_(gip[j] + bip[j]);
+        float ov = sig_(gop[j] + bop[j]);
+        float uv = tanh_(gup[j] + bup[j]);
+        float c  = iv * uv + fpp[j];
+        cvp[j] = c;
+        hvp[j] = ov * tanh_(c);
+      }
+      *(float4*)(a.CupA + (long)p * 512 + hq) = cv;
+      *(float4*)(&Hl[p * 512 + hq]) = hv;
+    }
+    __syncthreads();
+    if (tid < 128) {
+      int hq = tid << 2;
+      float4 s = {0.f, 0.f, 0.f, 0.f};
+#pragma unroll
+      for (int b = 0; b < 16; ++b) {
+        float4 v = *(const float4*)(&Hl[b * 512 + hq]);
+        s.x += v.x; s.y += v.y; s.z += v.z; s.w += v.w;
+      }
+      *(ushort4*)(a.xhC + hq) = *(const ushort4*)(a.Xbf + hq);
+      ushort4 hw = {f2bf(s.x), f2bf(s.y), f2bf(s.z), f2bf(s.w)};
+      *(ushort4*)(a.xhC + 512 + hq) = hw;
+    }
+  }
+  gbar(a.bar);
+
+  for (int bj = blockIdx.x; bj < 2432; bj += NBLK) {
+    int wid = bj * 4 + wave;
+    if (wid < 1536) {
+      const uint16_t* ap = a.xhC;
+      const uint16_t* bp = a.Wg + (long)wid * 1024;
+      int k0 = lane * 16;
+      float s = 0.f;
+#pragma unroll
+      for (int j = 0; j < 16; j += 4) {
+        ushort4 avv = *(const ushort4*)(ap + k0 + j);
+        ushort4 bvv = *(const ushort4*)(bp + k0 + j);
+        s += bf2f(avv.x) * bf2f(bvv.x) + bf2f(avv.y) * bf2f(bvv.y)
+           + bf2f(avv.z) * bf2f(bvv.z) + bf2f(avv.w) * bf2f(bvv.w);
+      }
+#pragma unroll
+      for (int off = 32; off; off >>= 1) s += __shfl_xor(s, off, 64);
+      if (lane == 0) a.Gf[wid] = s;
+    } else {
+      int w2 = wid - 1536;
+      int m = w2 >> 9, n = w2 & 511;
+      const float* ap = a.CupA + (long)m * 512;
+      const float* bp = a.WfF + (long)n * 1024;
+      int k0 = lane * 8;
+      float s = 0.f;
+#pragma unroll
+      for (int j = 0; j < 8; j += 4) {
+        float4 avv = *(const float4*)(ap + k0 + j);
+        float4 bvv = *(const float4*)(bp + k0 + j);
+        s += avv.x * bvv.x + avv.y * bvv.y + avv.z * bvv.z + avv.w * bvv.w;
+      }
+#pragma unroll
+      for (int off = 32; off; off >>= 1) s += __shfl_xor(s, off, 64);
+      if (lane == 0) a.Fc[(long)m * 512 + n] = s;
+    }
+  }
+  gbar(a.bar);
+
+  if (blockIdx.x == 0 && tid < 128) {
+    int hq = tid << 2;
+    float4 fxv = *(const float4*)(a.FxAll + hq);
+    float4 bfv = *(const float4*)(a.bfb + hq);
+    float fx0 = fxv.x + bfv.x, fx1 = fxv.y + bfv.y;
+    float fx2 = fxv.z + bfv.z, fx3 = fxv.w + bfv.w;
+    float a0 = 0.f, a1 = 0.f, a2 = 0.f, a3 = 0.f;
+#pragma unroll 4
+    for (int b = 0; b < 16; ++b) {
+      float4 f = *(const float4*)(a.Fc + (long)b * 512 + hq);
+      float4 c = *(const float4*)(a.CupA + (long)b * 512 + hq);
+      a0 += sig_(fx0 + f.x) * c.x;
+      a1 += sig_(fx1 + f.y) * c.y;
+      a2 += sig_(fx2 + f.z) * c.z;
+      a3 += sig_(fx3 + f.w) * c.w;
+    }
+    float fpp[4] = {a0, a1, a2, a3};
+    float4 gi = *(const float4*)(a.Gf + hq);
+    float4 go = *(const float4*)(a.Gf + 512 + hq);
+    float4 gu = *(const float4*)(a.Gf + 1024 + hq);
+    float4 b_i = *(const float4*)(a.bi + hq);
+    float4 b_o = *(const float4*)(a.bo + hq);
+    float4 b_u = *(const float4*)(a.bu + hq);
     const float* gip = &gi.x; const float* gop = &go.x;
     const float* gup = &gu.x; const float* bip = &b_i.x;
     const float* bop = &b_o.x; const float* bup = &b_u.x;
-    const float* fpp = &fp.x;
     float4 hv, cv;
     float* hvp = &hv.x; float* cvp = &cv.x;
 #pragma unroll
@@ -726,70 +792,9 @@
       cvp[j] = c;
       hvp[j] = ov * tanh_(c);
     }
-    *(float4*)(Cv + (long)p * 512 + hq) = cv;
-    *(float4*)(&Hl[p * 512 + hq]) = hv;
-  }
-  __syncthreads();
-  if (tid < 128) {
-    int hq = tid << 2;
-    float4 s = {0.f, 0.f, 0.f, 0.f};
-#pragma unroll
-    for (int b = 0; b < 16; ++b) {
-      float4 v = *(const float4*)(&Hl[b * 512 + hq]);
-      s.x += v.x; s.y += v.y; s.z += v.z; s.w += v.w;
-    }
-    *(ushort4*)(xh + hq) = *(const ushort4*)(xroot + hq);
-    ushort4 hw = {f2bf(s.x), f2bf(s.y), f2bf(s.z), f2bf(s.w)};
-    *(ushort4*)(xh + 512 + hq) = hw;
-  }
-}
-
-__global__ void k_root_tail(const float* __restrict__ Fc,
-                            const float* __restrict__ Fx,
-                            const float* __restrict__ bfb,
-                            const float* __restrict__ Cc,
-                            const float* __restrict__ G,
-                            const float* __restrict__ bi,
-                            const float* __restrict__ bo,
-                            const float* __restrict__ bu,
-                            float* __restrict__ H, float* __restrict__ Cv) {
-  int hq = (threadIdx.x & 127) << 2;
-  float4 fxv = *(const float4*)(Fx + hq);
-  float4 bfv = *(const float4*)(bfb + hq);
-  float fx0 = fxv.x + bfv.x, fx1 = fxv.y + bfv.y;
-  float fx2 = fxv.z + bfv.z, fx3 = fxv.w + bfv.w;
-  float a0 = 0.f, a1 = 0.f, a2 = 0.f, a3 = 0.f;
-#pragma unroll 4
-  for (int b = 0; b < 16; ++b) {
-    float4 f = *(const float4*)(Fc + (long)b * 512 + hq);
-    float4 c = *(const float4*)(Cc + (long)b * 512 + hq);
-    a0 += sig_(fx0 + f.x) * c.x;
-    a1 += sig_(fx1 + f.y) * c.y;
-    a2 += sig_(fx2 + f.z) * c.z;
-    a3 += sig_(fx3 + f.w) * c.w;
-  }
-  float fpp[4] = {a0, a1, a2, a3};
-  float4 gi = *(const float4*)(G + hq);
-  float4 go = *(const float4*)(G + 512 + hq);
-  float4 gu = *(const float4*)(G + 1024 + hq);
-  float4 b_i = *(const float4*)(bi + hq);
-  float4 b_o = *(const float4*)(bo + hq);
-  float4 b_u = *(const float4*)(bu + hq);
-  const float* gip = &gi.x; const float* gop = &go.x; const float* gup = &gu.x;
-  const float* bip = &b_i.x; const float* bop = &b_o.x; const float* bup = &b_u.x;
-  float4 hv, cv;
-  float* hvp = &hv.x; float* cvp = &cv.x;
-#pragma unroll
-  for (int j = 0; j < 4; ++j) {
-    float iv = sig_(gip[j] + bip[j]);
-    float ov = sig_(gop[j] + bop[j]);
-    float uv = tanh_(gup[j] + bup[j]);
-    float c  = iv * uv + fpp[j];
-    cvp[j] = c;
-    hvp[j] = ov * tanh_(c);
-  }
-  *(float4*)(H  + hq) = hv;
-  *(float4*)(Cv + hq) = cv;
+    *(float4*)(a.H  + hq) = hv;
+    *(float4*)(a.Cv + hq) = cv;
+  }
 }
 
 extern "C" void kernel_launch(void* const* d_in, const int* in_sizes, int n_in,
@@ -832,6 +837,9 @@
   float*    Gf    = (float*)alloc((size_t)16 * 1536 * 4);
   float*    Fc    = (float*)alloc((size_t)16 * 512 * 4);
   float*    CupA  = (float*)alloc((size_t)16 * 512 * 4);
+  unsigned* bar   = (unsigned*)alloc(256);
+
+  hipMemsetAsync(bar, 0, 2 * sizeof(unsigned), stream);
 
   {
     long n4x = NTOT * 512 / 4;
@@ -846,33 +854,13 @@
       Cbf, Xbf + offs[3] * 512, xhA,
       Xbf, Wf, FxAll);
 
-  k_fc4_l3g<<<2560, 256, 0, stream>>>(
-      Cbf, Wf + 512, FxAll + offs[3] * 512, wf_b, Fpart,
-      xhA, Wg, G3);
-
-  k_level_final<<<256, 128, 0, stream>>>(
-      G3, Fpart, wi_b, wo_b, wu_b, CbfU, Xbf + offs[2] * 512, xhB);
-
-  k_fc2_l2g<<<288, 256, 0, stream>>>(
-      CbfU, Wf + 512, FxAll + offs[2] * 512, wf_b, Fpart,
-      xhB, Wg, G3);
-
-  k_level_final<<<16, 128, 0, stream>>>(
-      G3, Fpart, wi_b, wo_b, wu_b, CbfU2, Xbf + offs[1] * 512, xhC);
-
-  k_fcdot<<<6160, 256, 0, stream>>>(CbfU2, Wf + 512,
-                                    FxAll + offs[1] * 512, wf_b, Fpart,
-                                    xhC, Wg, Gf);
-
-  k_lvl1_tail<<<1, 1024, 0, stream>>>(Gf, Fpart, wi_b, wo_b, wu_b,
-                                      CupA, Xbf + offs[0] * 512, xhC);
-
-  {
-    long waves = 1536 + 16L * 512;
-    k_dot_merge<<<(int)(waves / 4), 256, 0, stream>>>(
-        xhC, Wg, Gf, CupA, wf_w + 512, Fc);
-  }
-  k_root_tail<<<1, 128, 0, stream>>>(Fc, FxAll, wf_b, CupA, Gf,
-                                     wi_b, wo_b, wu_b,
-                                     (float*)d_out, (float*)d_out + 512);
-}
+  CoopArgs ca;
+  ca.Cbf = Cbf; ca.Wfc = Wf + 512; ca.FxAll = FxAll; ca.bfb = wf_b;
+  ca.Fpart = Fpart; ca.xhA = xhA; ca.Wg = Wg; ca.G3 = G3;
+  ca.bi = wi_b; ca.bo = wo_b; ca.bu = wu_b;
+  ca.CbfU = CbfU; ca.Xbf = Xbf; ca.xhB = xhB; ca.CbfU2 = CbfU2;
+  ca.xhC = xhC; ca.Gf = Gf; ca.CupA = CupA; ca.WfF = wf_w + 512;
+  ca.Fc = Fc; ca.H = (float*)d_out; ca.Cv = (float*)d_out + 512;
+  ca.bar = bar;
+  k_coop<<<NBLK, 256, 0, stream>>>(ca);
+}
```

New measurement: 1.562 ms. 230% more time.
